# Kernel optimization log

Measured on AMD Instinct MI355X. Metric: run time of the kernel, lower is better.

The kernel has to match this reference:

```python
import jax, jax.numpy as jnp
import numpy as np

V, E, H2, K = 50000, 64, 128, 3
H = H2 // 2  # per-direction LSTM hidden
B, T = 256, 512


def setup_inputs() -> dict:
    key = jax.random.key(0)
    ks = jax.random.split(key, 12)
    s = 0.1
    return {
        "x": jax.random.randint(ks[0], (B, T), 0, V, dtype=jnp.int32),
        "y": jax.random.randint(ks[1], (B, T), 0, K, dtype=jnp.int32),
        "mask": jnp.ones((B, T), dtype=bool),
        "emb": jax.random.normal(ks[2], (V, E), jnp.float32) * s,
        "w_ih_f": jax.random.normal(ks[3], (4 * H, E), jnp.float32) * s,
        "w_hh_f": jax.random.normal(ks[4], (4 * H, H), jnp.float32) * s,
        "b_ih_f": jnp.zeros((4 * H,), jnp.float32),
        "b_hh_f": jnp.zeros((4 * H,), jnp.float32),
        "w_ih_b": jax.random.normal(ks[5], (4 * H, E), jnp.float32) * s,
        "w_hh_b": jax.random.normal(ks[6], (4 * H, H), jnp.float32) * s,
        "b_ih_b": jnp.zeros((4 * H,), jnp.float32),
        "b_hh_b": jnp.zeros((4 * H,), jnp.float32),
        "fc_w": jax.random.normal(ks[7], (K, H2), jnp.float32) * s,
        "fc_b": jnp.zeros((K,), jnp.float32),
        "start_t": jax.random.normal(ks[8], (K,), jnp.float32) * s,
        "end_t": jax.random.normal(ks[9], (K,), jnp.float32) * s,
        "trans": jax.random.normal(ks[10], (K, K), jnp.float32) * s,
    }


def _lstm(x_tbe, w_ih, w_hh, b_ih, b_hh):
    # x_tbe: [T,B,E] -> hidden states [T,B,H]; torch gate order i,f,g,o
    pre = jnp.einsum('tbe,ge->tbg', x_tbe, w_ih) + b_ih + b_hh  # [T,B,4H]
    Bb = x_tbe.shape[1]
    Hh = w_hh.shape[1]

    def step(carry, p):
        h, c = carry
        g = p + h @ w_hh.T
        i, f, gg, o = jnp.split(g, 4, axis=-1)
        c = jax.nn.sigmoid(f) * c + jax.nn.sigmoid(i) * jnp.tanh(gg)
        h = jax.nn.sigmoid(o) * jnp.tanh(c)
        return (h, c), h

    init = (jnp.zeros((Bb, Hh), pre.dtype), jnp.zeros((Bb, Hh), pre.dtype))
    _, hs = jax.lax.scan(step, init, pre)
    return hs


def _emissions(x, emb, w_ih_f, w_hh_f, b_ih_f, b_hh_f,
               w_ih_b, w_hh_b, b_ih_b, b_hh_b, fc_w, fc_b):
    h = emb[x]                      # [B,T,E]
    h = jnp.swapaxes(h, 0, 1)       # [T,B,E] (time-major)
    hf = _lstm(h, w_ih_f, w_hh_f, b_ih_f, b_hh_f)            # [T,B,H]
    hb = _lstm(h[::-1], w_ih_b, w_hh_b, b_ih_b, b_hh_b)[::-1]  # [T,B,H]
    out = jnp.concatenate([hf, hb], axis=-1)                 # [T,B,2H]
    return jnp.einsum('tbh,kh->tbk', out, fc_w) + fc_b       # [T,B,K]


def _crf_nll(em, y, mask, start_t, end_t, trans):
    # em: [T,B,K]; y, mask: [B,T]. Returns -mean log-likelihood (torchcrf, reduction='mean').
    y_t = y.T                      # [T,B]
    m = mask.T.astype(em.dtype)    # [T,B]
    Bb = y_t.shape[1]
    bar = jnp.arange(Bb)
    # numerator (gold path score)
    score = start_t[y_t[0]] + em[0, bar, y_t[0]]
    trans_sc = trans[y_t[:-1], y_t[1:]]                                 # [T-1,B]
    em_sc = jnp.take_along_axis(em, y_t[..., None], axis=-1)[..., 0]    # [T,B]
    score = score + jnp.sum(m[1:] * (trans_sc + em_sc[1:]), axis=0)
    seq_ends = mask.T.astype(jnp.int32).sum(axis=0) - 1                 # [B]
    last_tags = y_t[seq_ends, bar]
    numerator = score + end_t[last_tags]
    # log-partition via forward algorithm (scan over time, K=3 states)
    alpha0 = start_t[None, :] + em[0]   # [B,K]

    def step(alpha, inp):
        em_i, m_i = inp
        nxt = jax.nn.logsumexp(alpha[:, :, None] + trans[None] + em_i[:, None, :], axis=1)
        return jnp.where(m_i[:, None] > 0, nxt, alpha), None

    alpha, _ = jax.lax.scan(step, alpha0, (em[1:], m[1:]))
    logZ = jax.nn.logsumexp(alpha + end_t[None, :], axis=1)   # [B]
    llh = numerator - logZ
    return -jnp.mean(llh)


def reference(x, y, mask, emb, w_ih_f, w_hh_f, b_ih_f, b_hh_f,
              w_ih_b, w_hh_b, b_ih_b, b_hh_b, fc_w, fc_b,
              start_t, end_t, trans):
    em = _emissions(x, emb, w_ih_f, w_hh_f, b_ih_f, b_hh_f,
                    w_ih_b, w_hh_b, b_ih_b, b_hh_b, fc_w, fc_b)
    return _crf_nll(em, y, mask, start_t, end_t, trans)
```

## Files before the change

kernel.cpp:

```cpp
#include <hip/hip_runtime.h>
#include <hip/hip_fp16.h>

static constexpr int TT = 512;
static constexpr int BB = 256;
static constexpr int EE = 64;
static constexpr int HH = 64;
static constexpr int KK = 3;

typedef _Float16 hv2   __attribute__((ext_vector_type(2)));
typedef _Float16 half8 __attribute__((ext_vector_type(8)));
typedef float    f32x4 __attribute__((ext_vector_type(4)));
typedef int      i32x4 __attribute__((ext_vector_type(4)));

__device__ __forceinline__ hv2 bch2(int u) { return __builtin_bit_cast(hv2, u); }
__device__ __forceinline__ hv2 rlh2(int v, int l) {
  return __builtin_bit_cast(hv2, __builtin_amdgcn_readlane(v, l));
}
__device__ __forceinline__ unsigned pk(float a, float b) {
  return __builtin_bit_cast(unsigned, __builtin_amdgcn_cvt_pkrtz(a, b));
}
__device__ __forceinline__ float lse3(float x0, float x1, float x2) {
  float m = fmaxf(fmaxf(x0, x1), x2);
  return m + __logf(__expf(x0 - m) + __expf(x1 - m) + __expf(x2 - m));
}
__device__ __forceinline__ void lds_barrier() {
  __asm__ volatile("s_waitcnt lgkmcnt(0)\n\ts_barrier" ::: "memory");
}

#define MFMA16(A, B, C) __builtin_amdgcn_mfma_f32_16x16x32_f16(A, B, C, 0, 0, 0)

#define LWF(dstv, row, src, kslice) { \
    const float* base = (src) + (size_t)(row) * 64 + 32 * (kslice) + quad * 8; \
    float4 u = *(const float4*)base; float4 v = *(const float4*)(base + 4); \
    i32x4 iv = {(int)pk(u.x, u.y), (int)pk(u.z, u.w), \
                (int)pk(v.x, v.y), (int)pk(v.z, v.w)}; \
    dstv = __builtin_bit_cast(half8, iv); }

#define TRSEL(ypv, ycv) ((ypv) == 0 ? ((ycv) == 0 ? t00 : (ycv) == 1 ? t01 : t02) \
                       : (ypv) == 1 ? ((ycv) == 0 ? t10 : (ycv) == 1 ? t11 : t12) \
                       :              ((ycv) == 0 ? t20 : (ycv) == 1 ? t21 : t22))

__global__ __launch_bounds__(512, 1) void lstm_fused(
    const int* __restrict__ x, const float* __restrict__ emb,
    const float* __restrict__ w_ih_f, const float* __restrict__ b_ih_f,
    const float* __restrict__ b_hh_f,
    const float* __restrict__ w_ih_b, const float* __restrict__ b_ih_b,
    const float* __restrict__ b_hh_b,
    const float* __restrict__ w_hh_f, const float* __restrict__ w_hh_b,
    __half* __restrict__ h16) {
  const int tid  = threadIdx.x;
  const int wv   = tid >> 6;
  const int l    = tid & 63;
  const int quad = l >> 4;
  const int c    = l & 15;
  const int bg   = blockIdx.x & 63;
  const int dir  = blockIdx.x >> 6;
  const int b0   = bg * 4;
  const int dirb4 = dir * BB + b0;

  const float* whh = dir ? w_hh_b : w_hh_f;
  const float* wih = dir ? w_ih_b : w_ih_f;
  const float* bih = dir ? b_ih_b : b_ih_f;
  const float* bhh = dir ? b_hh_b : b_hh_f;

  __shared__ __align__(16) _Float16 hbuf[2][16][72];
  __shared__ __align__(16) unsigned preLDS[16 * 512];

  const int rowbase = 16 * (wv & 3) + c;
  const float* wsrc = (wv < 4) ? whh : wih;
  half8 B0, B1, B2, B3, B4, B5, B6, B7;
  LWF(B0, rowbase,       wsrc, 0) LWF(B1, rowbase,       wsrc, 1)
  LWF(B2, rowbase + 64,  wsrc, 0) LWF(B3, rowbase + 64,  wsrc, 1)
  LWF(B4, rowbase + 128, wsrc, 0) LWF(B5, rowbase + 128, wsrc, 1)
  LWF(B6, rowbase + 192, wsrc, 0) LWF(B7, rowbase + 192, wsrc, 1)
  const float bias0 = bih[rowbase]       + bhh[rowbase];
  const float bias1 = bih[rowbase + 64]  + bhh[rowbase + 64];
  const float bias2 = bih[rowbase + 128] + bhh[rowbase + 128];
  const float bias3 = bih[rowbase + 192] + bhh[rowbase + 192];

  for (int i = tid; i < 2 * 16 * 72 / 2; i += 512) ((unsigned*)hbuf)[i] = 0u;

  int xr0 = 0, xr1 = 0;
  float4 E0, E1, E2, E3, E4, E5, E6, E7;
  const int* xpb = x + (b0 + (c & 3)) * TT;

#define XLOAD(g) { \
    int t2a = (g) * 8 + (c >> 2);     if (t2a > 511) t2a = 511; \
    int t2b = (g) * 8 + 4 + (c >> 2); if (t2b > 511) t2b = 511; \
    xr0 = xpb[dir ? (511 - t2a) : t2a]; \
    xr1 = xpb[dir ? (511 - t2b) : t2b]; }

#define EMBISSUE() { \
    const float* ea = emb + ((size_t)xr0 << 6) + quad * 8; \
    E0 = *(const float4*)ea;        E1 = *(const float4*)(ea + 4); \
    E2 = *(const float4*)(ea + 32); E3 = *(const float4*)(ea + 36); \
    const float* eb = emb + ((size_t)xr1 << 6) + quad * 8; \
    E4 = *(const float4*)eb;        E5 = *(const float4*)(eb + 4); \
    E6 = *(const float4*)(eb + 32); E7 = *(const float4*)(eb + 36); }

#define PPASS(g, p, EA, EB, EC, ED) { \
    i32x4 v0 = {(int)pk(EA.x, EA.y), (int)pk(EA.z, EA.w), \
                (int)pk(EB.x, EB.y), (int)pk(EB.z, EB.w)}; \
    i32x4 v1 = {(int)pk(EC.x, EC.y), (int)pk(EC.z, EC.w), \
                (int)pk(ED.x, ED.y), (int)pk(ED.z, ED.w)}; \
    half8 xa0 = __builtin_bit_cast(half8, v0); \
    half8 xa1 = __builtin_bit_cast(half8, v1); \
    f32x4 p0 = {bias0, bias0, bias0, bias0}; \
    f32x4 p1 = {bias1, bias1, bias1, bias1}; \
    f32x4 p2 = {bias2, bias2, bias2, bias2}; \
    f32x4 p3 = {bias3, bias3, bias3, bias3}; \
    p0 = MFMA16(xa0, B0, p0); p0 = MFMA16(xa1, B1, p0); \
    p1 = MFMA16(xa0, B2, p1); p1 = MFMA16(xa1, B3, p1); \
    p2 = MFMA16(xa0, B4, p2); p2 = MFMA16(xa1, B5, p2); \
    p3 = MFMA16(xa0, B6, p3); p3 = MFMA16(xa1, B7, p3); \
    const int s_ = (g) * 8 + (p) * 4 + quad; \
    char* wp = (char*)preLDS + (s_ & 15) * 2048 + (wv & 3) * 512 + c * 8; \
    { uint2 o; o.x = pk(p0[0], p1[0]); o.y = pk(p2[0], p3[0]); \
      *(uint2*)(wp + 0 * 128) = o; } \
    { uint2 o; o.x = pk(p0[1], p1[1]); o.y = pk(p2[1], p3[1]); \
      *(uint2*)(wp + 1 * 128) = o; } \
    { uint2 o; o.x = pk(p0[2], p1[2]); o.y = pk(p2[2], p3[2]); \
      *(uint2*)(wp + 2 * 128) = o; } \
    { uint2 o; o.x = pk(p0[3], p1[3]); o.y = pk(p2[3], p3[3]); \
      *(uint2*)(wp + 3 * 128) = o; } }

  const bool hvalid = (c & 3) == 0;
  const int  hbi    = c >> 2;
  const int  u_first = (wv == 0) ? 4 : wv;
  const int  tsp0 = dir ? (TT - u_first) : (u_first - 1);
  __half* hptr = h16 + ((size_t)(dirb4 + hbi) * TT + tsp0) * 64;
  const int hstep = dir ? -256 : 256;
  const int gd = 16 * wv + c;

  const char* plc = (const char*)preLDS;
  const int loff8 = (wv & 3) * 512 + l * 8;
  int off0 = 4 * 2048 + loff8, off1 = 5 * 2048 + loff8;
  int off2 = 6 * 2048 + loff8, off3 = 7 * 2048 + loff8;

  if (wv >= 4) {
    XLOAD(0) EMBISSUE()
    PPASS(0, 0, E0, E1, E2, E3) PPASS(0, 1, E4, E5, E6, E7)
    XLOAD(1) EMBISSUE()
    PPASS(1, 0, E0, E1, E2, E3) PPASS(1, 1, E4, E5, E6, E7)
    XLOAD(2) EMBISSUE()
    XLOAD(3)
  }
  __syncthreads();

  uint2 P0 = {0, 0}, P1 = P0, P2 = P0, P3 = P0;
  if (wv < 4) {
    P0 = *(const uint2*)(plc + 0 * 2048 + loff8);
    P1 = *(const uint2*)(plc + 1 * 2048 + loff8);
    P2 = *(const uint2*)(plc + 2 * 2048 + loff8);
    P3 = *(const uint2*)(plc + 3 * 2048 + loff8);
  }

  float cs = 0.f;
  f32x4 a0 = {0.f, 0.f, 0.f, 0.f};
  f32x4 a1 = a0, a2 = a0, a3 = a0;

#define CSTEP(st, BK) { \
    const int nb = ((st) + 1) & 1; \
    { hv2 p0 = bch2((int)P##BK.x), p1 = bch2((int)P##BK.y); \
      a0[0] = (float)p0.x; a1[0] = (float)p0.y; \
      a2[0] = (float)p1.x; a3[0] = (float)p1.y; } \
    P##BK = *(const uint2*)(plc + off##BK); \
    off##BK = (off##BK + 8192) & 32767; \
    const half8 ha0 = *(const half8*)&hbuf[(st) & 1][c][quad * 8]; \
    const half8 ha1 = *(const half8*)&hbuf[(st) & 1][c][32 + quad * 8]; \
    if (wv == ((st) & 3) && hvalid && (((st) != 0) || ci)) { \
      *(half8*)(hptr + quad * 8)      = ha0; \
      *(half8*)(hptr + 32 + quad * 8) = ha1; \
      hptr += hstep; } \
    a0 = MFMA16(ha0, B0, a0); a1 = MFMA16(ha0, B2, a1); \
    a2 = MFMA16(ha0, B4, a2); a3 = MFMA16(ha0, B6, a3); \
    a0 = MFMA16(ha1, B1, a0); a1 = MFMA16(ha1, B3, a1); \
    a2 = MFMA16(ha1, B5, a2); a3 = MFMA16(ha1, B7, a3); \
    { float iv = a0[0], fv = a1[0], gv = a2[0], ov = a3[0]; \
      float ef = __expf(-fv); \
      float sf = __builtin_amdgcn_rcpf(1.f + ef); \
      float ei = __expf(-iv); \
      float eg = __expf(-2.f * gv); \
      float itg = (1.f - eg) * __builtin_amdgcn_rcpf((1.f + ei) * (1.f + eg)); \
      float cn = sf * cs + itg; \
      float eo = __expf(-ov); \
      float ec = __expf(-2.f * cn); \
      float hn = (1.f - ec) * __builtin_amdgcn_rcpf((1.f + eo) * (1.f + ec)); \
      cs = cn; \
      hbuf[nb][quad * 4][gd] = (_Float16)hn; } }

  for (int ci = 0; ci < 64; ++ci) {
    if (wv < 4) CSTEP(0, 0)
    lds_barrier();
    if (wv < 4) CSTEP(1, 1) else PPASS(ci + 2, 0, E0, E1, E2, E3)
    lds_barrier();
    if (wv < 4) CSTEP(2, 2)
    lds_barrier();
    if (wv < 4) CSTEP(3, 3)
    lds_barrier();
    if (wv < 4) CSTEP(4, 0) else PPASS(ci + 2, 1, E4, E5, E6, E7)
    lds_barrier();
    if (wv < 4) CSTEP(5, 1) else EMBISSUE()
    lds_barrier();
    if (wv < 4) CSTEP(6, 2) else XLOAD(ci + 4)
    lds_barrier();
    if (wv < 4) CSTEP(7, 3)
    lds_barrier();
  }

  if (wv == 3 && hvalid) {
    const half8 hf0 = *(const half8*)&hbuf[0][c][quad * 8];
    const half8 hf1 = *(const half8*)&hbuf[0][c][32 + quad * 8];
    int tsl = dir ? 0 : (TT - 1);
    __half* dst = h16 + ((size_t)(dirb4 + hbi) * TT + tsl) * 64;
    *(half8*)(dst + quad * 8)      = hf0;
    *(half8*)(dst + 32 + quad * 8) = hf1;
  }
}

__global__ void emis_kernel(
    const __half* __restrict__ h16, const float* __restrict__ fc_w,
    const float* __restrict__ fc_b, float4* __restrict__ em4) {
  const int b   = blockIdx.x & 255;
  const int th  = blockIdx.x >> 8;
  const int tid = threadIdx.x;
  const int l   = tid & 63;

  int T0, T1, T2;
  { float2 v0 = *(const float2*)&fc_w[0 * 128 + 2 * l];
    float2 v1 = *(const float2*)&fc_w[1 * 128 + 2 * l];
    float2 v2 = *(const float2*)&fc_w[2 * 128 + 2 * l];
    T0 = (int)pk(v0.x, v0.y); T1 = (int)pk(v1.x, v1.y); T2 = (int)pk(v2.x, v2.y); }
  const float fb0 = fc_b[0], fb1 = fc_b[1], fb2 = fc_b[2];

  const int t = th * 256 + tid;
  const uint4* hf = (const uint4*)(h16 + ((size_t)b * TT + t) * 64);
  const uint4* hb = (const uint4*)(h16 + ((size_t)(BB + b) * TT + t) * 64);
  float a0 = fb0, a1 = fb1, a2 = fb2;
#define EMDOT(v, jbase) { \
    a0 = __builtin_amdgcn_fdot2(bch2((int)(v)), rlh2(T0, (jbase)), a0, false); \
    a1 = __builtin_amdgcn_fdot2(bch2((int)(v)), rlh2(T1, (jbase)), a1, false); \
    a2 = __builtin_amdgcn_fdot2(bch2((int)(v)), rlh2(T2, (jbase)), a2, false); }
#pragma unroll
  for (int cidx = 0; cidx < 8; ++cidx) {
    uint4 v = hf[cidx];
    EMDOT(v.x, cidx * 4 + 0) EMDOT(v.y, cidx * 4 + 1)
    EMDOT(v.z, cidx * 4 + 2) EMDOT(v.w, cidx * 4 + 3)
  }
#pragma unroll
  for (int cidx = 0; cidx < 8; ++cidx) {
    uint4 v = hb[cidx];
    EMDOT(v.x, 32 + cidx * 4 + 0) EMDOT(v.y, 32 + cidx * 4 + 1)
    EMDOT(v.z, 32 + cidx * 4 + 2) EMDOT(v.w, 32 + cidx * 4 + 3)
  }
  float4 o; o.x = a0; o.y = a1; o.z = a2; o.w = 0.f;
  em4[(size_t)t * BB + b] = o;
}

__global__ __launch_bounds__(256, 1) void crf_chunks(
    const int* __restrict__ y, const float4* __restrict__ em4,
    const float* __restrict__ trans, float4* __restrict__ cw4) {
  const int c = blockIdx.x;
  const int b = threadIdx.x;
  __shared__ float tr[9];
  if (threadIdx.x < 9) tr[threadIdx.x] = trans[threadIdx.x];
  __syncthreads();
  const float t00 = tr[0], t01 = tr[1], t02 = tr[2];
  const float t10 = tr[3], t11 = tr[4], t12 = tr[5];
  const float t20 = tr[6], t21 = tr[7], t22 = tr[8];

  const int t0 = (c == 0) ? 1 : c * 8;
  const int te = c * 8 + 8;
  const int* yb = y + (size_t)b * TT;

  float4 e = em4[(size_t)t0 * BB + b];
  float m00 = t00 + e.x, m01 = t01 + e.y, m02 = t02 + e.z;
  float m10 = t10 + e.x, m11 = t11 + e.y, m12 = t12 + e.z;
  float m20 = t20 + e.x, m21 = t21 + e.y, m22 = t22 + e.z;
  int yp = yb[t0 - 1];
  int yc = yb[t0];
  float sc = TRSEL(yp, yc) + (yc == 0 ? e.x : yc == 1 ? e.y : e.z);
  yp = yc;

  for (int t = t0 + 1; t < te; ++t) {
    float4 et = em4[(size_t)t * BB + b];
    float n00 = et.x + lse3(m00 + t00, m01 + t10, m02 + t20);
    float n01 = et.y + lse3(m00 + t01, m01 + t11, m02 + t21);
    float n02 = et.z + lse3(m00 + t02, m01 + t12, m02 + t22);
    float n10 = et.x + lse3(m10 + t00, m11 + t10, m12 + t20);
    float n11 = et.y + lse3(m10 + t01, m11 + t11, m12 + t21);
    float n12 = et.z + lse3(m10 + t02, m11 + t12, m12 + t22);
    float n20 = et.x + lse3(m20 + t00, m21 + t10, m22 + t20);
    float n21 = et.y + lse3(m20 + t01, m21 + t11, m22 + t21);
    float n22 = et.z + lse3(m20 + t02, m21 + t12, m22 + t22);
    m00 = n00; m01 = n01; m02 = n02;
    m10 = n10; m11 = n11; m12 = n12;
    m20 = n20; m21 = n21; m22 = n22;
    yc = yb[t];
    sc += TRSEL(yp, yc) + (yc == 0 ? et.x : yc == 1 ? et.y : et.z);
    yp = yc;
  }

  float4 o0 = {m00, m01, m02, m10};
  float4 o1 = {m11, m12, m20, m21};
  float4 o2 = {m22, sc, 0.f, 0.f};
  cw4[(size_t)(c * 3 + 0) * BB + b] = o0;
  cw4[(size_t)(c * 3 + 1) * BB + b] = o1;
  cw4[(size_t)(c * 3 + 2) * BB + b] = o2;
}

__global__ __launch_bounds__(64, 1) void crf_combine(
    const int* __restrict__ y, const float4* __restrict__ em4,
    const float4* __restrict__ cw4,
    const float* __restrict__ start_t, const float* __restrict__ end_t,
    float* __restrict__ out) {
  const int tid = threadIdx.x;
  const int b   = blockIdx.x * 64 + tid;

  const float s0 = start_t[0], s1 = start_t[1], s2 = start_t[2];
  const float en0 = end_t[0], en1 = end_t[1], en2 = end_t[2];
  const int* yb = y + (size_t)b * TT;

  float4 e0 = em4[b];
  const int y0 = yb[0], yl = yb[TT - 1];
  float a0 = s0 + e0.x, a1 = s1 + e0.y, a2 = s2 + e0.z;
  float score = (y0 == 0 ? s0 : y0 == 1 ? s1 : s2) +
                (y0 == 0 ? e0.x : y0 == 1 ? e0.y : e0.z) +
                (yl == 0 ? en0 : yl == 1 ? en1 : en2);

  float4 A0 = cw4[b], A1 = cw4[BB + b], A2 = cw4[2 * BB + b];
  for (int c = 0; c < 64; ++c) {
    float4 B0 = A0, B1 = A1, B2 = A2;
    if (c < 63) {
      const size_t base = (size_t)((c + 1) * 3) * BB + b;
      B0 = cw4[base]; B1 = cw4[base + BB]; B2 = cw4[base + 2 * BB];
    }
    score += A2.y;
    float na0 = lse3(a0 + A0.x, a1 + A0.w, a2 + A1.z);
    float na1 = lse3(a0 + A0.y, a1 + A1.x, a2 + A1.w);
    float na2 = lse3(a0 + A0.z, a1 + A1.y, a2 + A2.x);
    a0 = na0; a1 = na1; a2 = na2;
    A0 = B0; A1 = B1; A2 = B2;
  }

  const float logZ = lse3(a0 + en0, a1 + en1, a2 + en2);
  float llh = score - logZ;
#pragma unroll
  for (int m = 32; m >= 1; m >>= 1) llh += __shfl_xor(llh, m, 64);
  if (tid == 0) atomicAdd(out, -llh * (1.0f / 256.0f));
}

extern "C" void kernel_launch(void* const* d_in, const int* in_sizes, int n_in,
                              void* d_out, int out_size, void* d_ws, size_t ws_size,
                              hipStream_t stream) {
  const int*   x      = (const int*)d_in[0];
  const int*   y      = (const int*)d_in[1];
  const float* emb    = (const float*)d_in[3];
  const float* w_ih_f = (const float*)d_in[4];
  const float* w_hh_f = (const float*)d_in[5];
  const float* b_ih_f = (const float*)d_in[6];
  const float* b_hh_f = (const float*)d_in[7];
  const float* w_ih_b = (const float*)d_in[8];
  const float* w_hh_b = (const float*)d_in[9];
  const float* b_ih_b = (const float*)d_in[10];
  const float* b_hh_b = (const float*)d_in[11];
  const float* fc_w   = (const float*)d_in[12];
  const float* fc_b   = (const float*)d_in[13];
  const float* start_t= (const float*)d_in[14];
  const float* end_t  = (const float*)d_in[15];
  const float* trans  = (const float*)d_in[16];

  float* out = (float*)d_out;
  hipMemsetAsync(d_out, 0, sizeof(float), stream);

  const size_t h16_bytes = (size_t)2 * BB * TT * 64 * 2;
  const size_t em4_bytes = (size_t)TT * BB * 16;
  __half* h16 = (__half*)d_ws;
  float4* em4 = (float4*)((char*)d_ws + h16_bytes);
  float4* cw4 = (float4*)((char*)d_ws + h16_bytes + em4_bytes);

  lstm_fused<<<128, 512, 0, stream>>>(x, emb, w_ih_f, b_ih_f, b_hh_f,
                                      w_ih_b, b_ih_b, b_hh_b,
                                      w_hh_f, w_hh_b, h16);
  emis_kernel<<<512, 256, 0, stream>>>(h16, fc_w, fc_b, em4);
  crf_chunks<<<64, 256, 0, stream>>>(y, em4, trans, cw4);
  crf_combine<<<4, 64, 0, stream>>>(y, em4, cw4, start_t, end_t, out);
}
```

Baseline: 290.1 us.

## Fuse emissions, CRF chunk scan and combine into one kernel with last-block reduction

```diff
diff --git a/kernel.cpp b/kernel.cpp
--- a/kernel.cpp
+++ b/kernel.cpp
@@ -47,7 +47,7 @@
     const float* __restrict__ w_ih_b, const float* __restrict__ b_ih_b,
     const float* __restrict__ b_hh_b,
     const float* __restrict__ w_hh_f, const float* __restrict__ w_hh_b,
-    __half* __restrict__ h16) {
+    __half* __restrict__ h16, unsigned* __restrict__ cnt) {
   const int tid  = threadIdx.x;
   const int wv   = tid >> 6;
   const int l    = tid & 63;
@@ -57,6 +57,8 @@
   const int dir  = blockIdx.x >> 6;
   const int b0   = bg * 4;
   const int dirb4 = dir * BB + b0;
+
+  if (blockIdx.x == 0 && tid == 0) *cnt = 0u;
 
   const float* whh = dir ? w_hh_b : w_hh_f;
   const float* wih = dir ? w_ih_b : w_ih_f;
@@ -218,13 +220,38 @@
   }
 }
 
-__global__ void emis_kernel(
-    const __half* __restrict__ h16, const float* __restrict__ fc_w,
-    const float* __restrict__ fc_b, float4* __restrict__ em4) {
-  const int b   = blockIdx.x & 255;
-  const int th  = blockIdx.x >> 8;
-  const int tid = threadIdx.x;
-  const int l   = tid & 63;
+#define EMDOT(v, jbase) { \
+    e0 = __builtin_amdgcn_fdot2(bch2((int)(v)), rlh2(T0, (jbase)), e0, false); \
+    e1 = __builtin_amdgcn_fdot2(bch2((int)(v)), rlh2(T1, (jbase)), e1, false); \
+    e2 = __builtin_amdgcn_fdot2(bch2((int)(v)), rlh2(T2, (jbase)), e2, false); }
+
+#define EMIS_AT(t) { \
+    const uint4* hf = (const uint4*)(h16 + ((size_t)b * TT + (t)) * 64); \
+    const uint4* hb = (const uint4*)(h16 + ((size_t)(BB + b) * TT + (t)) * 64); \
+    e0 = fb0; e1 = fb1; e2 = fb2; \
+    _Pragma("unroll") \
+    for (int cidx = 0; cidx < 8; ++cidx) { \
+      uint4 v = hf[cidx]; \
+      EMDOT(v.x, cidx * 4 + 0) EMDOT(v.y, cidx * 4 + 1) \
+      EMDOT(v.z, cidx * 4 + 2) EMDOT(v.w, cidx * 4 + 3) \
+    } \
+    _Pragma("unroll") \
+    for (int cidx = 0; cidx < 8; ++cidx) { \
+      uint4 v = hb[cidx]; \
+      EMDOT(v.x, 32 + cidx * 4 + 0) EMDOT(v.y, 32 + cidx * 4 + 1) \
+      EMDOT(v.z, 32 + cidx * 4 + 2) EMDOT(v.w, 32 + cidx * 4 + 3) \
+    } }
+
+__global__ __launch_bounds__(256, 1) void crf_all(
+    const int* __restrict__ y, const __half* __restrict__ h16,
+    const float* __restrict__ fc_w, const float* __restrict__ fc_b,
+    const float* __restrict__ trans,
+    const float* __restrict__ start_t, const float* __restrict__ end_t,
+    float4* __restrict__ cw4, float4* __restrict__ em0,
+    unsigned* __restrict__ cnt, float* __restrict__ out) {
+  const int cix = blockIdx.x;
+  const int b   = threadIdx.x;
+  const int l   = b & 63;
 
   int T0, T1, T2;
   { float2 v0 = *(const float2*)&fc_w[0 * 128 + 2 * l];
@@ -233,99 +260,77 @@
     T0 = (int)pk(v0.x, v0.y); T1 = (int)pk(v1.x, v1.y); T2 = (int)pk(v2.x, v2.y); }
   const float fb0 = fc_b[0], fb1 = fc_b[1], fb2 = fc_b[2];
 
-  const int t = th * 256 + tid;
-  const uint4* hf = (const uint4*)(h16 + ((size_t)b * TT + t) * 64);
-  const uint4* hb = (const uint4*)(h16 + ((size_t)(BB + b) * TT + t) * 64);
-  float a0 = fb0, a1 = fb1, a2 = fb2;
-#define EMDOT(v, jbase) { \
-    a0 = __builtin_amdgcn_fdot2(bch2((int)(v)), rlh2(T0, (jbase)), a0, false); \
-    a1 = __builtin_amdgcn_fdot2(bch2((int)(v)), rlh2(T1, (jbase)), a1, false); \
-    a2 = __builtin_amdgcn_fdot2(bch2((int)(v)), rlh2(T2, (jbase)), a2, false); }
-#pragma unroll
-  for (int cidx = 0; cidx < 8; ++cidx) {
-    uint4 v = hf[cidx];
-    EMDOT(v.x, cidx * 4 + 0) EMDOT(v.y, cidx * 4 + 1)
-    EMDOT(v.z, cidx * 4 + 2) EMDOT(v.w, cidx * 4 + 3)
-  }
-#pragma unroll
-  for (int cidx = 0; cidx < 8; ++cidx) {
-    uint4 v = hb[cidx];
-    EMDOT(v.x, 32 + cidx * 4 + 0) EMDOT(v.y, 32 + cidx * 4 + 1)
-    EMDOT(v.z, 32 + cidx * 4 + 2) EMDOT(v.w, 32 + cidx * 4 + 3)
-  }
-  float4 o; o.x = a0; o.y = a1; o.z = a2; o.w = 0.f;
-  em4[(size_t)t * BB + b] = o;
-}
-
-__global__ __launch_bounds__(256, 1) void crf_chunks(
-    const int* __restrict__ y, const float4* __restrict__ em4,
-    const float* __restrict__ trans, float4* __restrict__ cw4) {
-  const int c = blockIdx.x;
-  const int b = threadIdx.x;
   __shared__ float tr[9];
+  __shared__ int lastflag;
+  __shared__ float red[4];
   if (threadIdx.x < 9) tr[threadIdx.x] = trans[threadIdx.x];
   __syncthreads();
   const float t00 = tr[0], t01 = tr[1], t02 = tr[2];
   const float t10 = tr[3], t11 = tr[4], t12 = tr[5];
   const float t20 = tr[6], t21 = tr[7], t22 = tr[8];
 
-  const int t0 = (c == 0) ? 1 : c * 8;
-  const int te = c * 8 + 8;
   const int* yb = y + (size_t)b * TT;
-
-  float4 e = em4[(size_t)t0 * BB + b];
-  float m00 = t00 + e.x, m01 = t01 + e.y, m02 = t02 + e.z;
-  float m10 = t10 + e.x, m11 = t11 + e.y, m12 = t12 + e.z;
-  float m20 = t20 + e.x, m21 = t21 + e.y, m22 = t22 + e.z;
-  int yp = yb[t0 - 1];
-  int yc = yb[t0];
-  float sc = TRSEL(yp, yc) + (yc == 0 ? e.x : yc == 1 ? e.y : e.z);
+  const int t0 = cix * 8;
+  float e0, e1, e2;
+
+  if (cix == 0) {
+    EMIS_AT(0)
+    float4 o = {e0, e1, e2, 0.f};
+    em0[b] = o;
+  }
+  const int ti = (cix == 0) ? 1 : t0;
+  EMIS_AT(ti)
+  float m00 = t00 + e0, m01 = t01 + e1, m02 = t02 + e2;
+  float m10 = t10 + e0, m11 = t11 + e1, m12 = t12 + e2;
+  float m20 = t20 + e0, m21 = t21 + e1, m22 = t22 + e2;
+  int yp = yb[ti - 1];
+  int yc = yb[ti];
+  float sc = TRSEL(yp, yc) + (yc == 0 ? e0 : yc == 1 ? e1 : e2);
   yp = yc;
 
-  for (int t = t0 + 1; t < te; ++t) {
-    float4 et = em4[(size_t)t * BB + b];
-    float n00 = et.x + lse3(m00 + t00, m01 + t10, m02 + t20);
-    float n01 = et.y + lse3(m00 + t01, m01 + t11, m02 + t21);
-    float n02 = et.z + lse3(m00 + t02, m01 + t12, m02 + t22);
-    float n10 = et.x + lse3(m10 + t00, m11 + t10, m12 + t20);
-    float n11 = et.y + lse3(m10 + t01, m11 + t11, m12 + t21);
-    float n12 = et.z + lse3(m10 + t02, m11 + t12, m12 + t22);
-    float n20 = et.x + lse3(m20 + t00, m21 + t10, m22 + t20);
-    float n21 = et.y + lse3(m20 + t01, m21 + t11, m22 + t21);
-    float n22 = et.z + lse3(m20 + t02, m21 + t12, m22 + t22);
+  for (int t = ti + 1; t < t0 + 8; ++t) {
+    EMIS_AT(t)
+    float n00 = e0 + lse3(m00 + t00, m01 + t10, m02 + t20);
+    float n01 = e1 + lse3(m00 + t01, m01 + t11, m02 + t21);
+    float n02 = e2 + lse3(m00 + t02, m01 + t12, m02 + t22);
+    float n10 = e0 + lse3(m10 + t00, m11 + t10, m12 + t20);
+    float n11 = e1 + lse3(m10 + t01, m11 + t11, m12 + t21);
+    float n12 = e2 + lse3(m10 + t02, m11 + t12, m12 + t22);
+    float n20 = e0 + lse3(m20 + t00, m21 + t10, m22 + t20);
+    float n21 = e1 + lse3(m20 + t01, m21 + t11, m22 + t21);
+    float n22 = e2 + lse3(m20 + t02, m21 + t12, m22 + t22);
     m00 = n00; m01 = n01; m02 = n02;
     m10 = n10; m11 = n11; m12 = n12;
     m20 = n20; m21 = n21; m22 = n22;
     yc = yb[t];
-    sc += TRSEL(yp, yc) + (yc == 0 ? et.x : yc == 1 ? et.y : et.z);
+    sc += TRSEL(yp, yc) + (yc == 0 ? e0 : yc == 1 ? e1 : e2);
     yp = yc;
   }
 
-  float4 o0 = {m00, m01, m02, m10};
-  float4 o1 = {m11, m12, m20, m21};
-  float4 o2 = {m22, sc, 0.f, 0.f};
-  cw4[(size_t)(c * 3 + 0) * BB + b] = o0;
-  cw4[(size_t)(c * 3 + 1) * BB + b] = o1;
-  cw4[(size_t)(c * 3 + 2) * BB + b] = o2;
-}
-
-__global__ __launch_bounds__(64, 1) void crf_combine(
-    const int* __restrict__ y, const float4* __restrict__ em4,
-    const float4* __restrict__ cw4,
-    const float* __restrict__ start_t, const float* __restrict__ end_t,
-    float* __restrict__ out) {
-  const int tid = threadIdx.x;
-  const int b   = blockIdx.x * 64 + tid;
+  { float4 o0 = {m00, m01, m02, m10};
+    float4 o1 = {m11, m12, m20, m21};
+    float4 o2 = {m22, sc, 0.f, 0.f};
+    cw4[(size_t)(cix * 3 + 0) * BB + b] = o0;
+    cw4[(size_t)(cix * 3 + 1) * BB + b] = o1;
+    cw4[(size_t)(cix * 3 + 2) * BB + b] = o2; }
+
+  __threadfence();
+  if (threadIdx.x == 0) {
+    unsigned old = atomicAdd(cnt, 1u);
+    lastflag = (old == 63u);
+  }
+  __syncthreads();
+  if (!lastflag) return;
+  __threadfence();
 
   const float s0 = start_t[0], s1 = start_t[1], s2 = start_t[2];
   const float en0 = end_t[0], en1 = end_t[1], en2 = end_t[2];
-  const int* yb = y + (size_t)b * TT;
-
-  float4 e0 = em4[b];
+
+  float4 ee = em0[b];
   const int y0 = yb[0], yl = yb[TT - 1];
-  float a0 = s0 + e0.x, a1 = s1 + e0.y, a2 = s2 + e0.z;
+  float a0v = s0 + ee.x, a1v = s1 + ee.y, a2v = s2 + ee.z;
   float score = (y0 == 0 ? s0 : y0 == 1 ? s1 : s2) +
-                (y0 == 0 ? e0.x : y0 == 1 ? e0.y : e0.z) +
+                (y0 == 0 ? ee.x : y0 == 1 ? ee.y : ee.z) +
                 (yl == 0 ? en0 : yl == 1 ? en1 : en2);
 
   float4 A0 = cw4[b], A1 = cw4[BB + b], A2 = cw4[2 * BB + b];
@@ -336,18 +341,21 @@
       B0 = cw4[base]; B1 = cw4[base + BB]; B2 = cw4[base + 2 * BB];
     }
     score += A2.y;
-    float na0 = lse3(a0 + A0.x, a1 + A0.w, a2 + A1.z);
-    float na1 = lse3(a0 + A0.y, a1 + A1.x, a2 + A1.w);
-    float na2 = lse3(a0 + A0.z, a1 + A1.y, a2 + A2.x);
-    a0 = na0; a1 = na1; a2 = na2;
+    float na0 = lse3(a0v + A0.x, a1v + A0.w, a2v + A1.z);
+    float na1 = lse3(a0v + A0.y, a1v + A1.x, a2v + A1.w);
+    float na2 = lse3(a0v + A0.z, a1v + A1.y, a2v + A2.x);
+    a0v = na0; a1v = na1; a2v = na2;
     A0 = B0; A1 = B1; A2 = B2;
   }
 
-  const float logZ = lse3(a0 + en0, a1 + en1, a2 + en2);
+  const float logZ = lse3(a0v + en0, a1v + en1, a2v + en2);
   float llh = score - logZ;
 #pragma unroll
   for (int m = 32; m >= 1; m >>= 1) llh += __shfl_xor(llh, m, 64);
-  if (tid == 0) atomicAdd(out, -llh * (1.0f / 256.0f));
+  if (l == 0) red[threadIdx.x >> 6] = llh;
+  __syncthreads();
+  if (threadIdx.x == 0)
+    *out = -(red[0] + red[1] + red[2] + red[3]) * (1.0f / 256.0f);
 }
 
 extern "C" void kernel_launch(void* const* d_in, const int* in_sizes, int n_in,
@@ -371,18 +379,18 @@
   const float* trans  = (const float*)d_in[16];
 
   float* out = (float*)d_out;
-  hipMemsetAsync(d_out, 0, sizeof(float), stream);
 
   const size_t h16_bytes = (size_t)2 * BB * TT * 64 * 2;
-  const size_t em4_bytes = (size_t)TT * BB * 16;
-  __half* h16 = (__half*)d_ws;
-  float4* em4 = (float4*)((char*)d_ws + h16_bytes);
-  float4* cw4 = (float4*)((char*)d_ws + h16_bytes + em4_bytes);
+  const size_t cw4_bytes = (size_t)64 * 3 * BB * 16;
+  const size_t em0_bytes = (size_t)BB * 16;
+  __half*   h16 = (__half*)d_ws;
+  float4*   cw4 = (float4*)((char*)d_ws + h16_bytes);
+  float4*   em0 = (float4*)((char*)d_ws + h16_bytes + cw4_bytes);
+  unsigned* cnt = (unsigned*)((char*)d_ws + h16_bytes + cw4_bytes + em0_bytes);
 
   lstm_fused<<<128, 512, 0, stream>>>(x, emb, w_ih_f, b_ih_f, b_hh_f,
                                       w_ih_b, b_ih_b, b_hh_b,
-                                      w_hh_f, w_hh_b, h16);
-  emis_kernel<<<512, 256, 0, stream>>>(h16, fc_w, fc_b, em4);
-  crf_chunks<<<64, 256, 0, stream>>>(y, em4, trans, cw4);
-  crf_combine<<<4, 64, 0, stream>>>(y, em4, cw4, start_t, end_t, out);
-}
+                                      w_hh_f, w_hh_b, h16, cnt);
+  crf_all<<<64, 256, 0, stream>>>(y, h16, fc_w, fc_b, trans,
+                                  start_t, end_t, cw4, em0, cnt, out);
+}
```

After: 299.4 us. +3.2%, slower.

## Split LSTM MFMA accumulation into two chains and fuse CRF kernels via last-block counter

Applied to the files above, without the earlier changes.

```diff
diff --git a/kernel.cpp b/kernel.cpp
--- a/kernel.cpp
+++ b/kernel.cpp
@@ -47,7 +47,7 @@
     const float* __restrict__ w_ih_b, const float* __restrict__ b_ih_b,
     const float* __restrict__ b_hh_b,
     const float* __restrict__ w_hh_f, const float* __restrict__ w_hh_b,
-    __half* __restrict__ h16) {
+    __half* __restrict__ h16, unsigned* __restrict__ cnt) {
   const int tid  = threadIdx.x;
   const int wv   = tid >> 6;
   const int l    = tid & 63;
@@ -57,6 +57,8 @@
   const int dir  = blockIdx.x >> 6;
   const int b0   = bg * 4;
   const int dirb4 = dir * BB + b0;
+
+  if (blockIdx.x == 0 && tid == 0) *cnt = 0u;
 
   const float* whh = dir ? w_hh_b : w_hh_f;
   const float* wih = dir ? w_ih_b : w_ih_f;
@@ -158,12 +160,14 @@
   float cs = 0.f;
   f32x4 a0 = {0.f, 0.f, 0.f, 0.f};
   f32x4 a1 = a0, a2 = a0, a3 = a0;
+  f32x4 b0v = a0, b1v = a0, b2v = a0, b3v = a0;
 
 #define CSTEP(st, BK) { \
     const int nb = ((st) + 1) & 1; \
     { hv2 p0 = bch2((int)P##BK.x), p1 = bch2((int)P##BK.y); \
       a0[0] = (float)p0.x; a1[0] = (float)p0.y; \
       a2[0] = (float)p1.x; a3[0] = (float)p1.y; } \
+    b0v[0] = 0.f; b1v[0] = 0.f; b2v[0] = 0.f; b3v[0] = 0.f; \
     P##BK = *(const uint2*)(plc + off##BK); \
     off##BK = (off##BK + 8192) & 32767; \
     const half8 ha0 = *(const half8*)&hbuf[(st) & 1][c][quad * 8]; \
@@ -172,11 +176,13 @@
       *(half8*)(hptr + quad * 8)      = ha0; \
       *(half8*)(hptr + 32 + quad * 8) = ha1; \
       hptr += hstep; } \
-    a0 = MFMA16(ha0, B0, a0); a1 = MFMA16(ha0, B2, a1); \
-    a2 = MFMA16(ha0, B4, a2); a3 = MFMA16(ha0, B6, a3); \
-    a0 = MFMA16(ha1, B1, a0); a1 = MFMA16(ha1, B3, a1); \
-    a2 = MFMA16(ha1, B5, a2); a3 = MFMA16(ha1, B7, a3); \
-    { float iv = a0[0], fv = a1[0], gv = a2[0], ov = a3[0]; \
+     \
+    a0  = MFMA16(ha0, B0, a0);  b0v = MFMA16(ha1, B1, b0v); \
+    a1  = MFMA16(ha0, B2, a1);  b1v = MFMA16(ha1, B3, b1v); \
+    a2  = MFMA16(ha0, B4, a2);  b2v = MFMA16(ha1, B5, b2v); \
+    a3  = MFMA16(ha0, B6, a3);  b3v = MFMA16(ha1, B7, b3v); \
+    { float iv = a0[0] + b0v[0], fv = a1[0] + b1v[0]; \
+      float gv = a2[0] + b2v[0], ov = a3[0] + b3v[0]; \
       float ef = __expf(-fv); \
       float sf = __builtin_amdgcn_rcpf(1.f + ef); \
       float ei = __expf(-iv); \
@@ -257,21 +263,28 @@
   em4[(size_t)t * BB + b] = o;
 }
 
-__global__ __launch_bounds__(256, 1) void crf_chunks(
+__global__ __launch_bounds__(256, 1) void crf_fused(
     const int* __restrict__ y, const float4* __restrict__ em4,
-    const float* __restrict__ trans, float4* __restrict__ cw4) {
-  const int c = blockIdx.x;
-  const int b = threadIdx.x;
+    const float* __restrict__ trans,
+    const float* __restrict__ start_t, const float* __restrict__ end_t,
+    float4* __restrict__ cw4, unsigned* __restrict__ cnt,
+    float* __restrict__ out) {
+  const int cix = blockIdx.x;
+  const int b   = threadIdx.x;
+  const int l   = b & 63;
+
   __shared__ float tr[9];
+  __shared__ int lastflag;
+  __shared__ float red[4];
   if (threadIdx.x < 9) tr[threadIdx.x] = trans[threadIdx.x];
   __syncthreads();
   const float t00 = tr[0], t01 = tr[1], t02 = tr[2];
   const float t10 = tr[3], t11 = tr[4], t12 = tr[5];
   const float t20 = tr[6], t21 = tr[7], t22 = tr[8];
 
-  const int t0 = (c == 0) ? 1 : c * 8;
-  const int te = c * 8 + 8;
   const int* yb = y + (size_t)b * TT;
+  const int t0 = (cix == 0) ? 1 : cix * 8;
+  const int te = cix * 8 + 8;
 
   float4 e = em4[(size_t)t0 * BB + b];
   float m00 = t00 + e.x, m01 = t01 + e.y, m02 = t02 + e.z;
@@ -301,53 +314,55 @@
     yp = yc;
   }
 
-  float4 o0 = {m00, m01, m02, m10};
-  float4 o1 = {m11, m12, m20, m21};
-  float4 o2 = {m22, sc, 0.f, 0.f};
-  cw4[(size_t)(c * 3 + 0) * BB + b] = o0;
-  cw4[(size_t)(c * 3 + 1) * BB + b] = o1;
-  cw4[(size_t)(c * 3 + 2) * BB + b] = o2;
-}
-
-__global__ __launch_bounds__(64, 1) void crf_combine(
-    const int* __restrict__ y, const float4* __restrict__ em4,
-    const float4* __restrict__ cw4,
-    const float* __restrict__ start_t, const float* __restrict__ end_t,
-    float* __restrict__ out) {
-  const int tid = threadIdx.x;
-  const int b   = blockIdx.x * 64 + tid;
+  { float4 o0 = {m00, m01, m02, m10};
+    float4 o1 = {m11, m12, m20, m21};
+    float4 o2 = {m22, sc, 0.f, 0.f};
+    cw4[(size_t)(cix * 3 + 0) * BB + b] = o0;
+    cw4[(size_t)(cix * 3 + 1) * BB + b] = o1;
+    cw4[(size_t)(cix * 3 + 2) * BB + b] = o2; }
+
+  __threadfence();
+  if (threadIdx.x == 0) {
+    unsigned old = atomicAdd(cnt, 1u);
+    lastflag = (old == 63u);
+  }
+  __syncthreads();
+  if (!lastflag) return;
+  __threadfence();
 
   const float s0 = start_t[0], s1 = start_t[1], s2 = start_t[2];
   const float en0 = end_t[0], en1 = end_t[1], en2 = end_t[2];
-  const int* yb = y + (size_t)b * TT;
-
-  float4 e0 = em4[b];
+
+  float4 ee = em4[b];
   const int y0 = yb[0], yl = yb[TT - 1];
-  float a0 = s0 + e0.x, a1 = s1 + e0.y, a2 = s2 + e0.z;
+  float a0v = s0 + ee.x, a1v = s1 + ee.y, a2v = s2 + ee.z;
   float score = (y0 == 0 ? s0 : y0 == 1 ? s1 : s2) +
-                (y0 == 0 ? e0.x : y0 == 1 ? e0.y : e0.z) +
+                (y0 == 0 ? ee.x : y0 == 1 ? ee.y : ee.z) +
                 (yl == 0 ? en0 : yl == 1 ? en1 : en2);
 
   float4 A0 = cw4[b], A1 = cw4[BB + b], A2 = cw4[2 * BB + b];
-  for (int c = 0; c < 64; ++c) {
+  for (int c2 = 0; c2 < 64; ++c2) {
     float4 B0 = A0, B1 = A1, B2 = A2;
-    if (c < 63) {
-      const size_t base = (size_t)((c + 1) * 3) * BB + b;
+    if (c2 < 63) {
+      const size_t base = (size_t)((c2 + 1) * 3) * BB + b;
       B0 = cw4[base]; B1 = cw4[base + BB]; B2 = cw4[base + 2 * BB];
     }
     score += A2.y;
-    float na0 = lse3(a0 + A0.x, a1 + A0.w, a2 + A1.z);
-    float na1 = lse3(a0 + A0.y, a1 + A1.x, a2 + A1.w);
-    float na2 = lse3(a0 + A0.z, a1 + A1.y, a2 + A2.x);
-    a0 = na0; a1 = na1; a2 = na2;
+    float na0 = lse3(a0v + A0.x, a1v + A0.w, a2v + A1.z);
+    float na1 = lse3(a0v + A0.y, a1v + A1.x, a2v + A1.w);
+    float na2 = lse3(a0v + A0.z, a1v + A1.y, a2v + A2.x);
+    a0v = na0; a1v = na1; a2v = na2;
     A0 = B0; A1 = B1; A2 = B2;
   }
 
-  const float logZ = lse3(a0 + en0, a1 + en1, a2 + en2);
+  const float logZ = lse3(a0v + en0, a1v + en1, a2v + en2);
   float llh = score - logZ;
 #pragma unroll
   for (int m = 32; m >= 1; m >>= 1) llh += __shfl_xor(llh, m, 64);
-  if (tid == 0) atomicAdd(out, -llh * (1.0f / 256.0f));
+  if (l == 0) red[threadIdx.x >> 6] = llh;
+  __syncthreads();
+  if (threadIdx.x == 0)
+    *out = -(red[0] + red[1] + red[2] + red[3]) * (1.0f / 256.0f);
 }
 
 extern "C" void kernel_launch(void* const* d_in, const int* in_sizes, int n_in,
@@ -371,18 +386,19 @@
   const float* trans  = (const float*)d_in[16];
 
   float* out = (float*)d_out;
-  hipMemsetAsync(d_out, 0, sizeof(float), stream);
 
   const size_t h16_bytes = (size_t)2 * BB * TT * 64 * 2;
   const size_t em4_bytes = (size_t)TT * BB * 16;
-  __half* h16 = (__half*)d_ws;
-  float4* em4 = (float4*)((char*)d_ws + h16_bytes);
-  float4* cw4 = (float4*)((char*)d_ws + h16_bytes + em4_bytes);
+  const size_t cw4_bytes = (size_t)64 * 3 * BB * 16;
+  __half*   h16 = (__half*)d_ws;
+  float4*   em4 = (float4*)((char*)d_ws + h16_bytes);
+  float4*   cw4 = (float4*)((char*)d_ws + h16_bytes + em4_bytes);
+  unsigned* cnt = (unsigned*)((char*)d_ws + h16_bytes + em4_bytes + cw4_bytes);
 
   lstm_fused<<<128, 512, 0, stream>>>(x, emb, w_ih_f, b_ih_f, b_hh_f,
                                       w_ih_b, b_ih_b, b_hh_b,
-                                      w_hh_f, w_hh_b, h16);
+                                      w_hh_f, w_hh_b, h16, cnt);
   emis_kernel<<<512, 256, 0, stream>>>(h16, fc_w, fc_b, em4);
-  crf_chunks<<<64, 256, 0, stream>>>(y, em4, trans, cw4);
-  crf_combine<<<4, 64, 0, stream>>>(y, em4, cw4, start_t, end_t, out);
-}
+  crf_fused<<<64, 256, 0, stream>>>(y, em4, trans, start_t, end_t,
+                                    cw4, cnt, out);
+}
```

New measurement: 297.6 us. +2.6%, slower.
